# Kernel tuning notes

Hardware: AMD Instinct MI355X
Metric: run time of the kernel (lower is better)

The kernel has to match this reference:

```python
import jax, jax.numpy as jnp
import numpy as np

CH = 256
HEADS = 8
WIN = (8, 16)
EPS = 1e-5


def layer_norm(x, g, b):
    mu = jnp.mean(x, axis=-1, keepdims=True)
    var = jnp.mean((x - mu) ** 2, axis=-1, keepdims=True)
    return (x - mu) * jax.lax.rsqrt(var + EPS) * g + b


def setup_inputs() -> dict:
    key = jax.random.key(0)
    ks = jax.random.split(key, 12)
    C = CH
    s = lambda n: 1.0 / np.sqrt(n)
    return {
        "x": jax.random.normal(ks[0], (4, C, 256, 256), jnp.float32),
        "w_qkv": jax.random.normal(ks[1], (C, 3 * C), jnp.float32) * s(C),
        "w_proj": jax.random.normal(ks[2], (C, C), jnp.float32) * s(C),
        "b_proj": jnp.zeros((C,), jnp.float32),
        "g1": jnp.ones((C,), jnp.float32),
        "b1": jnp.zeros((C,), jnp.float32),
        "g2": jnp.ones((C,), jnp.float32),
        "b2": jnp.zeros((C,), jnp.float32),
        "w_fc1": jax.random.normal(ks[3], (C, 4 * C), jnp.float32) * s(C),
        "b_fc1": jnp.zeros((4 * C,), jnp.float32),
        "w_fc2": jax.random.normal(ks[4], (4 * C, C), jnp.float32) * s(4 * C),
        "b_fc2": jnp.zeros((C,), jnp.float32),
    }


def reference(x, w_qkv, w_proj, b_proj, g1, b1, g2, b2, w_fc1, b_fc1, w_fc2, b_fc2):
    B, C, H, W = x.shape
    Ph, Pw = WIN
    pad_h = (Ph - H % Ph) % Ph
    pad_w = (Pw - W % Pw) % Pw
    x = jnp.pad(x, ((0, 0), (0, 0), (0, pad_h), (0, pad_w)))
    Hp, Wp = H + pad_h, W + pad_w
    # [B,C,Hp,Wp] -> windows [nw, Ph, Pw, C]
    xw = jnp.transpose(x, (0, 2, 3, 1))
    xw = xw.reshape(B, Hp // Ph, Ph, Wp // Pw, Pw, C)
    xw = jnp.transpose(xw, (0, 1, 3, 2, 4, 5)).reshape(-1, Ph, Pw, C)
    nw = xw.shape[0]
    N = Ph * Pw
    hd = C // HEADS
    # attention branch
    h = layer_norm(xw, g1, b1).reshape(nw, N, C)
    qkv = (h @ w_qkv).reshape(nw, N, 3, HEADS, hd)
    q = jnp.transpose(qkv[:, :, 0], (0, 2, 1, 3))  # [nw, heads, N, hd]
    k = jnp.transpose(qkv[:, :, 1], (0, 2, 1, 3))
    v = jnp.transpose(qkv[:, :, 2], (0, 2, 1, 3))
    attn = jnp.einsum('whnd,whmd->whnm', q, k) * (1.0 / np.sqrt(hd))
    attn = jax.nn.softmax(attn, axis=-1)
    out = jnp.einsum('whnm,whmd->whnd', attn, v)
    out = jnp.transpose(out, (0, 2, 1, 3)).reshape(nw, N, C)
    out = (out @ w_proj + b_proj).reshape(nw, Ph, Pw, C)
    xw = xw + out
    # MLP branch
    h = layer_norm(xw, g2, b2)
    h = jax.nn.gelu(h @ w_fc1 + b_fc1, approximate=False) @ w_fc2 + b_fc2
    xw = xw + h
    # reverse windows
    xw = xw.reshape(B, Hp // Ph, Wp // Pw, Ph, Pw, C)
    xw = jnp.transpose(xw, (0, 1, 3, 2, 4, 5)).reshape(B, Hp, Wp, C)
    xw = xw[:, :H, :W, :]
    return jnp.transpose(xw, (0, 3, 1, 2))
```

## Files before the change

kernel.cpp:

```cpp
#include <hip/hip_runtime.h>
#include <cstdint>
#include <cstddef>

typedef __attribute__((ext_vector_type(4))) float f32x4;
typedef __attribute__((ext_vector_type(8))) __bf16 bf16x8;
typedef __attribute__((ext_vector_type(8))) unsigned short u16x8;

__device__ __forceinline__ unsigned short f2bf(float f) {
  unsigned u = __builtin_bit_cast(unsigned, f);
  u += 0x7FFFu + ((u >> 16) & 1u);
  return (unsigned short)(u >> 16);
}

__device__ __forceinline__ unsigned pack2(float lo, float hi) {
  return (unsigned)f2bf(lo) | ((unsigned)f2bf(hi) << 16);
}

__device__ __forceinline__ unsigned pk_bf16(float lo, float hi) {
  unsigned r;
  asm("v_cvt_pk_bf16_f32 %0, %1, %2" : "=v"(r) : "v"(lo), "v"(hi));
  return r;
}

__device__ __forceinline__ float gelu_f(float x) {
  float u = x * (1.5957691216057308f + 0.07135481627f * x * x);
  return x / (1.f + __expf(-u));
}

__device__ __forceinline__ f32x4 mfma16(bf16x8 a, bf16x8 b, f32x4 c) {
  return __builtin_amdgcn_mfma_f32_16x16x32_bf16(a, b, c, 0, 0, 0);
}

__global__ __launch_bounds__(256) void wconv(const float* __restrict__ w,
                                             unsigned short* __restrict__ wt,
                                             int K, int N) {
  int i = blockIdx.x * 256 + threadIdx.x;
  int k = i / N, n = i % N;
  wt[(size_t)n * K + k] = f2bf(w[i]);
}

__global__ __launch_bounds__(256) void wconv_frag(const float* __restrict__ w,
                                                  unsigned short* __restrict__ wf,
                                                  int N, int kshift) {
  int t = blockIdx.x * 256 + threadIdx.x;
  int e = t & 7;
  int lane = (t >> 3) & 63;
  int tq2 = lane & 15, kp2 = lane >> 4;
  int k32 = (t >> 9) & ((1 << kshift) - 1);
  int colblk = t >> (9 + kshift);
  int col = colblk * 16 + tq2;
  int k = k32 * 32 + kp2 * 8 + e;
  wf[t] = f2bf(w[(size_t)k * N + col]);
}

__global__ __launch_bounds__(256) void win_part(const float* __restrict__ x,
                                                float* __restrict__ xw) {
  __shared__ float tile[64 * 33];
  const int id = blockIdx.x;
  const int cb = id & 7, xb = (id >> 3) & 3, y = (id >> 5) & 255, b = id >> 13;
  const int c0 = cb * 32, x0 = xb * 64;
  const int tid = threadIdx.x;
  const int px = tid & 63, cq = tid >> 6;
#pragma unroll
  for (int i = 0; i < 8; ++i) {
    int cl = i * 4 + cq;
    tile[px * 33 + cl] = x[(((size_t)b * 256 + c0 + cl) * 256 + y) * 256 + x0 + px];
  }
  __syncthreads();
  const int cc = tid & 31, tq2 = tid >> 5;
#pragma unroll
  for (int it = 0; it < 8; ++it) {
    int tk = it * 8 + tq2;
    int xg = x0 + tk;
    int wg = b * 512 + (y >> 3) * 16 + (xg >> 4);
    int n = (y & 7) * 16 + (xg & 15);
    xw[((size_t)wg * 128 + n) * 256 + c0 + cc] = tile[tk * 33 + cc];
  }
}

__global__ __launch_bounds__(256) void ln_kernel(const float* __restrict__ xin,
                                                 const float* __restrict__ g,
                                                 const float* __restrict__ b,
                                                 unsigned short* __restrict__ out) {
  const int tok = (blockIdx.x << 2) + (threadIdx.x >> 6);
  const int lane = threadIdx.x & 63;
  const float4* px = (const float4*)(xin + (size_t)tok * 256);
  float4 v = px[lane];
  float s = v.x + v.y + v.z + v.w;
  float sq = v.x * v.x + v.y * v.y + v.z * v.z + v.w * v.w;
#pragma unroll
  for (int m = 32; m >= 1; m >>= 1) {
    s += __shfl_xor(s, m);
    sq += __shfl_xor(sq, m);
  }
  float mu = s * 0.00390625f;
  float var = sq * 0.00390625f - mu * mu;
  float rstd = rsqrtf(var + 1e-5f);
  float4 gv = ((const float4*)g)[lane];
  float4 bv = ((const float4*)b)[lane];
  unsigned p0 = pk_bf16((v.x - mu) * rstd * gv.x + bv.x, (v.y - mu) * rstd * gv.y + bv.y);
  unsigned p1 = pk_bf16((v.z - mu) * rstd * gv.z + bv.z, (v.w - mu) * rstd * gv.w + bv.w);
  uint2 o; o.x = p0; o.y = p1;
  ((uint2*)(out + (size_t)tok * 256))[lane] = o;
}

__global__ __launch_bounds__(256) void attn_kernel(const unsigned short* __restrict__ qkv,
                                                   unsigned short* __restrict__ attn_out,
                                                   int wbase) {
  __shared__ unsigned short Vt[4][32 * 128];
  const int wid = threadIdx.x >> 6, lane = threadIdx.x & 63;
  const int wloc = blockIdx.x >> 1;
  const int h = ((blockIdx.x & 1) << 2) + wid;
  const int w = wbase + wloc;
  const int tq = lane & 15, kp = lane >> 4;
  const unsigned short* base = qkv + (size_t)wloc * 98304;
  unsigned short* vt = &Vt[wid][0];

#pragma unroll
  for (int it = 0; it < 8; ++it) {
    int chunk = it * 64 + lane;
    int tt = chunk >> 2, dg = chunk & 3;
    u16x8 v = *(const u16x8*)(base + (size_t)tt * 768 + 512 + h * 32 + dg * 8);
    int pi = ((tt >> 5) << 5) | (((tt >> 2) & 3) << 3) | (((tt >> 4) & 1) << 2) | (tt & 3);
    int c = pi >> 3, wi = pi & 7;
#pragma unroll
    for (int j = 0; j < 8; ++j) {
      int d = dg * 8 + j;
      vt[d * 128 + ((c ^ (d & 7)) << 3) + wi] = v[j];
    }
  }
  bf16x8 kf[8];
#pragma unroll
  for (int nj = 0; nj < 8; ++nj)
    kf[nj] = *(const bf16x8*)(base + (size_t)(nj * 16 + tq) * 768 + 256 + h * 32 + kp * 8);
  __syncthreads();
  bf16x8 vf[4][2];
#pragma unroll
  for (int kk = 0; kk < 4; ++kk)
#pragma unroll
    for (int n2 = 0; n2 < 2; ++n2) {
      int d = n2 * 16 + tq;
      int tc = kk * 4 + kp;
      vf[kk][n2] = *(const bf16x8*)&vt[d * 128 + ((tc ^ (d & 7)) << 3)];
    }

  const float sc = 0.17677669529663687f;
  f32x4 z = {0.f, 0.f, 0.f, 0.f};
#pragma unroll 1
  for (int mi = 0; mi < 8; ++mi) {
    bf16x8 qf = *(const bf16x8*)(base + (size_t)(mi * 16 + tq) * 768 + h * 32 + kp * 8);
    f32x4 s[8];
#pragma unroll
    for (int nj = 0; nj < 8; ++nj) s[nj] = mfma16(kf[nj], qf, z);
    float m = -3.0e38f;
#pragma unroll
    for (int nj = 0; nj < 8; ++nj)
#pragma unroll
      for (int r = 0; r < 4; ++r) m = fmaxf(m, s[nj][r]);
    m = fmaxf(m, __shfl_xor(m, 16));
    m = fmaxf(m, __shfl_xor(m, 32));
    float sm = 0.f;
#pragma unroll
    for (int nj = 0; nj < 8; ++nj)
#pragma unroll
      for (int r = 0; r < 4; ++r) {
        float e = __expf((s[nj][r] - m) * sc);
        s[nj][r] = e;
        sm += e;
      }
    sm += __shfl_xor(sm, 16);
    sm += __shfl_xor(sm, 32);
    float inv = 1.f / sm;
    f32x4 o0 = z, o1 = z;
#pragma unroll
    for (int kc = 0; kc < 4; ++kc) {
      const f32x4 sa = s[2 * kc], sb = s[2 * kc + 1];
      uint4 bb;
      bb.x = pack2(sa[0] * inv, sa[1] * inv);
      bb.y = pack2(sa[2] * inv, sa[3] * inv);
      bb.z = pack2(sb[0] * inv, sb[1] * inv);
      bb.w = pack2(sb[2] * inv, sb[3] * inv);
      bf16x8 pb = __builtin_bit_cast(bf16x8, bb);
      o0 = mfma16(vf[kc][0], pb, o0);
      o1 = mfma16(vf[kc][1], pb, o1);
    }
    unsigned short* op = attn_out + ((size_t)w * 128 + mi * 16 + tq) * 256 + h * 32 + (kp << 2);
    uint2 s0, s1;
    s0.x = pk_bf16(o0[0], o0[1]); s0.y = pk_bf16(o0[2], o0[3]);
    s1.x = pk_bf16(o1[0], o1[1]); s1.y = pk_bf16(o1[2], o1[3]);
    *(uint2*)op = s0;
    *(uint2*)(op + 16) = s1;
  }
}

__global__ __launch_bounds__(256, 2) void mlp_fused(
    const float* __restrict__ xw, const float* __restrict__ g2,
    const float* __restrict__ b2, const unsigned short* __restrict__ W1f,
    const float* __restrict__ b_fc1, const unsigned short* __restrict__ W2f,
    const float* __restrict__ b_fc2, float* __restrict__ out) {
  __shared__ unsigned short As[64 * 256];
  __shared__ unsigned short Hs[64 * 128];
  const int tid = threadIdx.x;
  const int lane = tid & 63, wid = tid >> 6;
  const int tq = lane & 15, kp = lane >> 4;
  const int r0 = blockIdx.x << 6;

  {
    float4 gv = ((const float4*)g2)[lane];
    float4 bv = ((const float4*)b2)[lane];
    const int g = lane >> 1;
#pragma unroll 1
    for (int it = 0; it < 16; ++it) {
      int row = it * 4 + wid;
      float4 v = ((const float4*)(xw + (size_t)(r0 + row) * 256))[lane];
      float s = v.x + v.y + v.z + v.w;
      float sq = v.x * v.x + v.y * v.y + v.z * v.z + v.w * v.w;
#pragma unroll
      for (int m = 32; m >= 1; m >>= 1) {
        s += __shfl_xor(s, m);
        sq += __shfl_xor(sq, m);
      }
      float mu = s * 0.00390625f;
      float var = sq * 0.00390625f - mu * mu;
      float rstd = rsqrtf(var + 1e-5f);
      uint2 st;
      st.x = pack2((v.x - mu) * rstd * gv.x + bv.x, (v.y - mu) * rstd * gv.y + bv.y);
      st.y = pack2((v.z - mu) * rstd * gv.z + bv.z, (v.w - mu) * rstd * gv.w + bv.w);
      int gs = (g & 24) | ((g & 7) ^ (row & 7));
      *(uint2*)&As[row * 256 + gs * 8 + (lane & 1) * 4] = st;
    }
  }
  __syncthreads();

  f32x4 acc2[4][4] = {};
#pragma unroll 1
  for (int cc = 0; cc < 8; ++cc) {
    bf16x8 bw1[8][2];
#pragma unroll
    for (int k32 = 0; k32 < 8; ++k32)
#pragma unroll
      for (int j = 0; j < 2; ++j) {
        int colblk = cc * 8 + wid * 2 + j;
        bw1[k32][j] = *(const bf16x8*)(W1f + (((size_t)colblk * 8 + k32) * 64 + lane) * 8);
      }
    __builtin_amdgcn_sched_barrier(0);
    f32x4 acc1[4][2] = {};
#pragma unroll
    for (int k32 = 0; k32 < 8; ++k32) {
      bf16x8 af[4];
#pragma unroll
      for (int i = 0; i < 4; ++i) {
        int row = i * 16 + tq;
        int g = k32 * 4 + kp;
        int gs = (g & 24) | ((g & 7) ^ (row & 7));
        af[i] = *(const bf16x8*)&As[row * 256 + gs * 8];
      }
#pragma unroll
      for (int j = 0; j < 2; ++j)
#pragma unroll
        for (int i = 0; i < 4; ++i) acc1[i][j] = mfma16(bw1[k32][j], af[i], acc1[i][j]);
    }
#pragma unroll
    for (int i = 0; i < 4; ++i)
#pragma unroll
      for (int j = 0; j < 2; ++j) {
        int row = i * 16 + tq;
        int col = wid * 32 + j * 16 + (kp << 2);
        f32x4 bb = *(const f32x4*)&b_fc1[cc * 128 + col];
        f32x4 a = acc1[i][j];
        uint2 st;
        st.x = pack2(gelu_f(a[0] + bb[0]), gelu_f(a[1] + bb[1]));
        st.y = pack2(gelu_f(a[2] + bb[2]), gelu_f(a[3] + bb[3]));
        int g = col >> 3;
        int gs = (g & 8) | ((g & 7) ^ (row & 7));
        *(uint2*)&Hs[row * 128 + gs * 8 + (col & 7)] = st;
      }
    bf16x8 bw2[4][4];
#pragma unroll
    for (int k32 = 0; k32 < 4; ++k32)
#pragma unroll
      for (int j = 0; j < 4; ++j) {
        int colblk = wid * 4 + j;
        bw2[k32][j] = *(const bf16x8*)(W2f + (((size_t)colblk * 32 + cc * 4 + k32) * 64 + lane) * 8);
      }
    __builtin_amdgcn_sched_barrier(0);
    __syncthreads();
#pragma unroll
    for (int k32 = 0; k32 < 4; ++k32) {
      bf16x8 ah[4];
#pragma unroll
      for (int i = 0; i < 4; ++i) {
        int row = i * 16 + tq;
        int g = k32 * 4 + kp;
        int gs = (g & 8) | ((g & 7) ^ (row & 7));
        ah[i] = *(const bf16x8*)&Hs[row * 128 + gs * 8];
      }
#pragma unroll
      for (int j = 0; j < 4; ++j)
#pragma unroll
        for (int i = 0; i < 4; ++i) acc2[i][j] = mfma16(ah[i], bw2[k32][j], acc2[i][j]);
    }
    __syncthreads();
  }

#pragma unroll
  for (int i = 0; i < 4; ++i) {
    const int rowbase = r0 + i * 16 + (kp << 2);
    const int wg = rowbase >> 7, n = rowbase & 127;
    const int bb_ = wg >> 9, wy = (wg >> 4) & 31, wx = wg & 15;
    const int y = wy * 8 + (n >> 4), xp = wx * 16 + (n & 15);
#pragma unroll
    for (int j = 0; j < 4; ++j) {
      const int colg = wid * 64 + j * 16 + tq;
      const size_t oidx = (((size_t)bb_ * 256 + colg) << 16) + (size_t)y * 256 + xp;
      const float bvv = b_fc2[colg];
      f32x4 v = acc2[i][j];
      f32x4 ov;
#pragma unroll
      for (int r = 0; r < 4; ++r)
        ov[r] = v[r] + bvv + xw[(size_t)(rowbase + r) * 256 + colg];
      *(f32x4*)(out + oidx) = ov;
    }
  }
}

template <int EPI>
__global__ __launch_bounds__(256) void gemm_bt(const unsigned short* __restrict__ A, int ldA,
                                               const unsigned short* __restrict__ Bt, int ldB,
                                               const float* __restrict__ bias,
                                               void* __restrict__ C, int ldC,
                                               int K) {
  __shared__ unsigned short As[128 * 64];
  __shared__ unsigned short Bs[128 * 64];
  const int tid = threadIdx.x;
  const int lane = tid & 63, wid = tid >> 6;
  const int wr = wid >> 1, wc = wid & 1;
  const int nbx = gridDim.x;
  const int nwg = nbx * gridDim.y;
  int id = blockIdx.y * nbx + blockIdx.x;
  if ((nwg & 7) == 0) id = (id & 7) * (nwg >> 3) + (id >> 3);
  const int m0 = (id / nbx) << 7, n0 = (id % nbx) << 7;
  f32x4 acc[4][4] = {};

  for (int k0 = 0; k0 < K; k0 += 64) {
    __syncthreads();
#pragma unroll
    for (int it = 0; it < 4; ++it) {
      int lc = it * 256 + tid;
      int row = lc >> 3, cch = lc & 7;
      int cs = cch ^ (row & 7);
      __builtin_amdgcn_global_load_lds(
          (const __attribute__((address_space(1))) unsigned int*)(A + (size_t)(m0 + row) * ldA + k0 + cs * 8),
          (__attribute__((address_space(3))) unsigned int*)(&As[lc * 8]), 16, 0, 0);
      __builtin_amdgcn_global_load_lds(
          (const __attribute__((address_space(1))) unsigned int*)(Bt + (size_t)(n0 + row) * ldB + k0 + cs * 8),
          (__attribute__((address_space(3))) unsigned int*)(&Bs[lc * 8]), 16, 0, 0);
    }
    __syncthreads();
#pragma unroll
    for (int kk = 0; kk < 2; ++kk) {
      bf16x8 af[4], bfr[4];
#pragma unroll
      for (int i = 0; i < 4; ++i) {
        int arow = wr * 64 + i * 16 + (lane & 15);
        int ach = (kk * 4 + (lane >> 4)) ^ (arow & 7);
        af[i] = *(const bf16x8*)&As[arow * 64 + ach * 8];
        int brow = wc * 64 + i * 16 + (lane & 15);
        int bch = (kk * 4 + (lane >> 4)) ^ (brow & 7);
        bfr[i] = *(const bf16x8*)&Bs[brow * 64 + bch * 8];
      }
#pragma unroll
      for (int i = 0; i < 4; ++i)
#pragma unroll
        for (int j = 0; j < 4; ++j)
          acc[i][j] = mfma16(bfr[j], af[i], acc[i][j]);
    }
  }

  const int r0 = m0 + wr * 64;
  const int c0 = n0 + wc * 64;
  const int rl = lane & 15, cq = (lane >> 4) << 2;
#pragma unroll
  for (int i = 0; i < 4; ++i) {
    const int rowg = r0 + i * 16 + rl;
#pragma unroll
    for (int j = 0; j < 4; ++j) {
      const int colg = c0 + j * 16 + cq;
      f32x4 v = acc[i][j];
      if constexpr (EPI == 0) {
        uint2 st;
        st.x = pk_bf16(v[0], v[1]);
        st.y = pk_bf16(v[2], v[3]);
        *(uint2*)((unsigned short*)C + (size_t)rowg * ldC + colg) = st;
      } else {
        float* cp = (float*)C + (size_t)rowg * ldC + colg;
        f32x4 old = *(const f32x4*)cp;
        f32x4 bv = *(const f32x4*)&bias[colg];
        *(f32x4*)cp = old + v + bv;
      }
    }
  }
}

extern "C" void kernel_launch(void* const* d_in, const int* in_sizes, int n_in,
                              void* d_out, int out_size, void* d_ws, size_t ws_size,
                              hipStream_t stream) {
  (void)in_sizes; (void)n_in; (void)out_size;
  const float* x = (const float*)d_in[0];
  const float* w_qkv = (const float*)d_in[1];
  const float* w_proj = (const float*)d_in[2];
  const float* b_proj = (const float*)d_in[3];
  const float* g1v = (const float*)d_in[4];
  const float* b1v = (const float*)d_in[5];
  const float* g2v = (const float*)d_in[6];
  const float* b2v = (const float*)d_in[7];
  const float* w_fc1 = (const float*)d_in[8];
  const float* b_fc1 = (const float*)d_in[9];
  const float* w_fc2 = (const float*)d_in[10];
  const float* b_fc2 = (const float*)d_in[11];
  float* out = (float*)d_out;
  char* ws = (char*)d_ws;

  const size_t FULL_NEED = 939524096ull + 1572864ull;
  const bool full = (ws_size >= FULL_NEED);

  size_t off_xw, off_h, off_qkv, off_attn, off_w;
  if (full) {
    off_xw = 0; off_h = 268435456ull; off_qkv = 402653184ull;
    off_attn = 805306368ull; off_w = 939524096ull;
  } else {
    off_xw = 0; off_qkv = 268435456ull; off_attn = 469762048ull;
    off_h = 603979776ull; off_w = 738197504ull;
  }
  float* xw = (float*)(ws + off_xw);
  unsigned short* hbuf = (unsigned short*)(ws + off_h);
  unsigned short* qkvb = (unsigned short*)(ws + off_qkv);
  unsigned short* attnb = (unsigned short*)(ws + off_attn);
  unsigned short* wqkvT = (unsigned short*)(ws + off_w);
  unsigned short* wprojT = (unsigned short*)(ws + off_w + 393216);
  unsigned short* wfc1F = (unsigned short*)(ws + off_w + 524288);
  unsigned short* wfc2F = (unsigned short*)(ws + off_w + 1048576);

  wconv<<<768, 256, 0, stream>>>(w_qkv, wqkvT, 256, 768);
  wconv<<<256, 256, 0, stream>>>(w_proj, wprojT, 256, 256);
  wconv_frag<<<1024, 256, 0, stream>>>(w_fc1, wfc1F, 1024, 3);
  wconv_frag<<<1024, 256, 0, stream>>>(w_fc2, wfc2F, 256, 5);
  win_part<<<32768, 256, 0, stream>>>(x, xw);
  ln_kernel<<<65536, 256, 0, stream>>>(xw, g1v, b1v, hbuf);

  if (full) {
    gemm_bt<0><<<dim3(6, 2048), 256, 0, stream>>>(hbuf, 256, wqkvT, 256, nullptr, qkvb, 768, 256);
    attn_kernel<<<4096, 256, 0, stream>>>(qkvb, attnb, 0);
  } else {
    for (int half = 0; half < 2; ++half) {
      gemm_bt<0><<<dim3(6, 1024), 256, 0, stream>>>(hbuf + (size_t)half * 131072 * 256, 256, wqkvT, 256,
                                                    nullptr, qkvb, 768, 256);
      attn_kernel<<<2048, 256, 0, stream>>>(qkvb, attnb, half * 1024);
    }
  }
  gemm_bt<1><<<dim3(2, 2048), 256, 0, stream>>>(attnb, 256, wprojT, 256, b_proj, xw, 256, 256);
  mlp_fused<<<4096, 256, 0, stream>>>(xw, g2v, b2v, wfc1F, b_fc1, wfc2F, b_fc2, out);
}
```

Before: 1.239 ms.

## Fuse LayerNorm1 into QKV GEMM and prefetch fc1 weight fragments

Replaces the standalone LayerNorm kernel and the generic QKV GEMM with one fused kernel. It normalizes a 64-token tile into swizzled LDS as bf16, then runs MFMA against pre-fragmented QKV weights, prefetching the next column chunk's weights during compute. This removes the bf16 intermediate write and re-read of the normalized activations and shrinks the workspace. The MLP kernel is also changed to load the next fc1 weight fragments ahead of time, which raises register pressure.

```diff
diff --git a/kernel.cpp b/kernel.cpp
--- a/kernel.cpp
+++ b/kernel.cpp
@@ -78,30 +78,92 @@
   }
 }
 
-__global__ __launch_bounds__(256) void ln_kernel(const float* __restrict__ xin,
-                                                 const float* __restrict__ g,
-                                                 const float* __restrict__ b,
-                                                 unsigned short* __restrict__ out) {
-  const int tok = (blockIdx.x << 2) + (threadIdx.x >> 6);
-  const int lane = threadIdx.x & 63;
-  const float4* px = (const float4*)(xin + (size_t)tok * 256);
-  float4 v = px[lane];
-  float s = v.x + v.y + v.z + v.w;
-  float sq = v.x * v.x + v.y * v.y + v.z * v.z + v.w * v.w;
-#pragma unroll
-  for (int m = 32; m >= 1; m >>= 1) {
-    s += __shfl_xor(s, m);
-    sq += __shfl_xor(sq, m);
-  }
-  float mu = s * 0.00390625f;
-  float var = sq * 0.00390625f - mu * mu;
-  float rstd = rsqrtf(var + 1e-5f);
-  float4 gv = ((const float4*)g)[lane];
-  float4 bv = ((const float4*)b)[lane];
-  unsigned p0 = pk_bf16((v.x - mu) * rstd * gv.x + bv.x, (v.y - mu) * rstd * gv.y + bv.y);
-  unsigned p1 = pk_bf16((v.z - mu) * rstd * gv.z + bv.z, (v.w - mu) * rstd * gv.w + bv.w);
-  uint2 o; o.x = p0; o.y = p1;
-  ((uint2*)(out + (size_t)tok * 256))[lane] = o;
+__global__ __launch_bounds__(256, 3) void qkv_fused(
+    const float* __restrict__ xw, const float* __restrict__ g1,
+    const float* __restrict__ b1, const unsigned short* __restrict__ Wf,
+    unsigned short* __restrict__ qkvb) {
+  __shared__ unsigned short As[64 * 256];
+  const int tid = threadIdx.x;
+  const int lane = tid & 63, wid = tid >> 6;
+  const int tq = lane & 15, kp = lane >> 4;
+  const int r0 = blockIdx.x << 6;
+
+  {
+    float4 gv = ((const float4*)g1)[lane];
+    float4 bv = ((const float4*)b1)[lane];
+    const int g = lane >> 1;
+#pragma unroll 1
+    for (int it = 0; it < 16; ++it) {
+      int row = it * 4 + wid;
+      float4 v = ((const float4*)(xw + (size_t)(r0 + row) * 256))[lane];
+      float s = v.x + v.y + v.z + v.w;
+      float sq = v.x * v.x + v.y * v.y + v.z * v.z + v.w * v.w;
+#pragma unroll
+      for (int m = 32; m >= 1; m >>= 1) {
+        s += __shfl_xor(s, m);
+        sq += __shfl_xor(sq, m);
+      }
+      float mu = s * 0.00390625f;
+      float var = sq * 0.00390625f - mu * mu;
+      float rstd = rsqrtf(var + 1e-5f);
+      uint2 st;
+      st.x = pack2((v.x - mu) * rstd * gv.x + bv.x, (v.y - mu) * rstd * gv.y + bv.y);
+      st.y = pack2((v.z - mu) * rstd * gv.z + bv.z, (v.w - mu) * rstd * gv.w + bv.w);
+      int gs = (g & 24) | ((g & 7) ^ (row & 7));
+      *(uint2*)&As[row * 256 + gs * 8 + (lane & 1) * 4] = st;
+    }
+  }
+  __syncthreads();
+
+  bf16x8 bw[8][2];
+#pragma unroll
+  for (int k32 = 0; k32 < 8; ++k32)
+#pragma unroll
+    for (int j = 0; j < 2; ++j) {
+      int colblk = wid * 2 + j;
+      bw[k32][j] = *(const bf16x8*)(Wf + (((size_t)colblk * 8 + k32) * 64 + lane) * 8);
+    }
+#pragma unroll 1
+  for (int cc = 0; cc < 6; ++cc) {
+    __builtin_amdgcn_sched_barrier(0);
+    f32x4 acc1[4][2] = {};
+#pragma unroll
+    for (int k32 = 0; k32 < 8; ++k32) {
+      bf16x8 af[4];
+#pragma unroll
+      for (int i = 0; i < 4; ++i) {
+        int row = i * 16 + tq;
+        int g = k32 * 4 + kp;
+        int gs = (g & 24) | ((g & 7) ^ (row & 7));
+        af[i] = *(const bf16x8*)&As[row * 256 + gs * 8];
+      }
+#pragma unroll
+      for (int j = 0; j < 2; ++j)
+#pragma unroll
+        for (int i = 0; i < 4; ++i) acc1[i][j] = mfma16(bw[k32][j], af[i], acc1[i][j]);
+    }
+    if (cc < 5) {
+#pragma unroll
+      for (int k32 = 0; k32 < 8; ++k32)
+#pragma unroll
+        for (int j = 0; j < 2; ++j) {
+          int colblk = (cc + 1) * 8 + wid * 2 + j;
+          bw[k32][j] = *(const bf16x8*)(Wf + (((size_t)colblk * 8 + k32) * 64 + lane) * 8);
+        }
+    }
+    __builtin_amdgcn_sched_barrier(0);
+#pragma unroll
+    for (int i = 0; i < 4; ++i)
+#pragma unroll
+      for (int j = 0; j < 2; ++j) {
+        int row = r0 + i * 16 + tq;
+        int col = cc * 128 + wid * 32 + j * 16 + (kp << 2);
+        uint2 st;
+        st.x = pk_bf16(acc1[i][j][0], acc1[i][j][1]);
+        st.y = pk_bf16(acc1[i][j][2], acc1[i][j][3]);
+        *(uint2*)(qkvb + (size_t)row * 768 + col) = st;
+      }
+  }
 }
 
 __global__ __launch_bounds__(256) void attn_kernel(const unsigned short* __restrict__ qkv,
@@ -232,17 +294,18 @@
   }
   __syncthreads();
 
+  bf16x8 bw1[8][2];
+#pragma unroll
+  for (int k32 = 0; k32 < 8; ++k32)
+#pragma unroll
+    for (int j = 0; j < 2; ++j) {
+      int colblk = wid * 2 + j;
+      bw1[k32][j] = *(const bf16x8*)(W1f + (((size_t)colblk * 8 + k32) * 64 + lane) * 8);
+    }
+
   f32x4 acc2[4][4] = {};
 #pragma unroll 1
   for (int cc = 0; cc < 8; ++cc) {
-    bf16x8 bw1[8][2];
-#pragma unroll
-    for (int k32 = 0; k32 < 8; ++k32)
-#pragma unroll
-      for (int j = 0; j < 2; ++j) {
-        int colblk = cc * 8 + wid * 2 + j;
-        bw1[k32][j] = *(const bf16x8*)(W1f + (((size_t)colblk * 8 + k32) * 64 + lane) * 8);
-      }
     __builtin_amdgcn_sched_barrier(0);
     f32x4 acc1[4][2] = {};
 #pragma unroll
@@ -283,6 +346,15 @@
         int colblk = wid * 4 + j;
         bw2[k32][j] = *(const bf16x8*)(W2f + (((size_t)colblk * 32 + cc * 4 + k32) * 64 + lane) * 8);
       }
+    if (cc < 7) {
+#pragma unroll
+      for (int k32 = 0; k32 < 8; ++k32)
+#pragma unroll
+        for (int j = 0; j < 2; ++j) {
+          int colblk = (cc + 1) * 8 + wid * 2 + j;
+          bw1[k32][j] = *(const bf16x8*)(W1f + (((size_t)colblk * 8 + k32) * 64 + lane) * 8);
+        }
+    }
     __builtin_amdgcn_sched_barrier(0);
     __syncthreads();
 #pragma unroll
@@ -421,40 +493,35 @@
   float* out = (float*)d_out;
   char* ws = (char*)d_ws;
 
-  const size_t FULL_NEED = 939524096ull + 1572864ull;
+  const size_t FULL_NEED = 805306368ull + 1572864ull;
   const bool full = (ws_size >= FULL_NEED);
 
-  size_t off_xw, off_h, off_qkv, off_attn, off_w;
+  size_t off_qkv, off_attn, off_w;
   if (full) {
-    off_xw = 0; off_h = 268435456ull; off_qkv = 402653184ull;
-    off_attn = 805306368ull; off_w = 939524096ull;
+    off_qkv = 268435456ull; off_attn = 671088640ull; off_w = 805306368ull;
   } else {
-    off_xw = 0; off_qkv = 268435456ull; off_attn = 469762048ull;
-    off_h = 603979776ull; off_w = 738197504ull;
-  }
-  float* xw = (float*)(ws + off_xw);
-  unsigned short* hbuf = (unsigned short*)(ws + off_h);
+    off_qkv = 268435456ull; off_attn = 469762048ull; off_w = 603979776ull;
+  }
+  float* xw = (float*)ws;
   unsigned short* qkvb = (unsigned short*)(ws + off_qkv);
   unsigned short* attnb = (unsigned short*)(ws + off_attn);
-  unsigned short* wqkvT = (unsigned short*)(ws + off_w);
+  unsigned short* wqkvF = (unsigned short*)(ws + off_w);
   unsigned short* wprojT = (unsigned short*)(ws + off_w + 393216);
   unsigned short* wfc1F = (unsigned short*)(ws + off_w + 524288);
   unsigned short* wfc2F = (unsigned short*)(ws + off_w + 1048576);
 
-  wconv<<<768, 256, 0, stream>>>(w_qkv, wqkvT, 256, 768);
+  wconv_frag<<<768, 256, 0, stream>>>(w_qkv, wqkvF, 768, 3);
   wconv<<<256, 256, 0, stream>>>(w_proj, wprojT, 256, 256);
   wconv_frag<<<1024, 256, 0, stream>>>(w_fc1, wfc1F, 1024, 3);
   wconv_frag<<<1024, 256, 0, stream>>>(w_fc2, wfc2F, 256, 5);
   win_part<<<32768, 256, 0, stream>>>(x, xw);
-  ln_kernel<<<65536, 256, 0, stream>>>(xw, g1v, b1v, hbuf);
 
   if (full) {
-    gemm_bt<0><<<dim3(6, 2048), 256, 0, stream>>>(hbuf, 256, wqkvT, 256, nullptr, qkvb, 768, 256);
+    qkv_fused<<<4096, 256, 0, stream>>>(xw, g1v, b1v, wqkvF, qkvb);
     attn_kernel<<<4096, 256, 0, stream>>>(qkvb, attnb, 0);
   } else {
     for (int half = 0; half < 2; ++half) {
-      gemm_bt<0><<<dim3(6, 1024), 256, 0, stream>>>(hbuf + (size_t)half * 131072 * 256, 256, wqkvT, 256,
-                                                    nullptr, qkvb, 768, 256);
+      qkv_fused<<<2048, 256, 0, stream>>>(xw + (size_t)half * 131072 * 256, g1v, b1v, wqkvF, qkvb);
       attn_kernel<<<2048, 256, 0, stream>>>(qkvb, attnb, half * 1024);
     }
   }
```

Result: faster. 1.176 ms (-5.1%).
